# Optimization experiments

Measured on AMD Instinct MI355X. Metric: run time of the kernel, lower is better.

Reference implementation:

```python
import jax, jax.numpy as jnp
import numpy as np

N_VISIBLE = 50000
N_HIDDEN = 5000
N_NODES = N_VISIBLE + N_HIDDEN
N_EDGES = 1_000_000
BATCH = 128


def setup_inputs() -> dict:
    key = jax.random.key(0)
    k1, k2, k3, k4, k5 = jax.random.split(key, 5)
    # parameters, initialized as in the torch module
    linear = 0.05 * (2.0 * jax.random.uniform(k1, (N_NODES,), dtype=jnp.float32) - 1.0)
    quadratic = 5.0 * (2.0 * jax.random.uniform(k2, (N_EDGES,), dtype=jnp.float32) - 1.0)
    # bipartite visible-hidden edges -> CSR-like flat buffers (via segment ids)
    flat_adj = jax.random.randint(k3, (N_EDGES,), 0, N_VISIBLE, dtype=jnp.int32).astype(jnp.int64)  # visible endpoint per edge
    seg_ids = jax.random.randint(k4, (N_EDGES,), 0, N_HIDDEN, dtype=jnp.int32).astype(jnp.int64)    # hidden bin per edge
    flat_j_idx = jnp.arange(N_EDGES, dtype=jnp.int64)  # quadratic coefficient index per flat entry
    hidden_idx = jnp.arange(N_HIDDEN, dtype=jnp.int64) + N_VISIBLE
    # observed spin configurations in {0,1} (mapped to +-1 inside reference)
    s = jax.random.randint(k5, (BATCH, N_NODES), 0, 2, dtype=jnp.int32)
    return {
        "linear": linear,
        "quadratic": quadratic,
        "s": s,
        "flat_adj": flat_adj,
        "flat_j_idx": flat_j_idx,
        "seg_ids": seg_ids,
        "hidden_idx": hidden_idx,
        "n_hidden": N_HIDDEN,
    }


def reference(linear, quadratic, s, flat_adj, flat_j_idx, seg_ids, hidden_idx, n_hidden):
    """Per-hidden-unit effective field + conditional spin expectation.

    eff[b, k] = linear[hidden_idx[k]]
                + sum_{e : seg_ids[e]==k} quadratic[flat_j_idx[e]] * s_pm[b, flat_adj[e]]
    returns tanh(-eff)  (conditional expectation of hidden spins given visibles)
    """
    s_pm = (2 * s - 1).astype(linear.dtype)                 # {0,1} -> {-1,+1}, (B, N)
    w = quadratic[flat_j_idx]                               # (E,)
    contrib = s_pm[:, flat_adj].T * w[:, None]              # (E, B) gathered neighbor terms
    field = jax.ops.segment_sum(contrib, seg_ids, num_segments=n_hidden)  # (K, B)
    eff = field.T + linear[hidden_idx][None, :]             # (B, K)
    return jnp.tanh(-eff)
```

## Files before the change

kernel.cpp:

```cpp
#include <hip/hip_runtime.h>
#include <math.h>
#include <stdint.h>

#define NV 50000
#define NH 5000
#define NN 55000
#define NCB 313
#define BCAP 4096
#define FSLOT 384
#define CHUNK 4096
#define SCAN_N 320


__global__ void __launch_bounds__(256) pack_zero_kernel(
        const int* __restrict__ s, uint32_t* __restrict__ bits,
        uint32_t* __restrict__ coarse_cnt) {
    if (blockIdx.x == 0)
        for (int i = threadIdx.x; i < NCB; i += 256) coarse_cnt[i] = 0u;
    int tid = blockIdx.x * 256 + threadIdx.x;
    int v = tid >> 2;
    int g = tid & 3;
    if (v >= NV) return;
    const int* col = s + (size_t)g * 32 * NN + v;
    uint32_t w = 0;
#pragma unroll
    for (int j = 0; j < 32; ++j)
        w |= (uint32_t)(col[(size_t)j * NN] & 1) << j;
    bits[(size_t)v * 4 + g] = w;
}

__global__ void __launch_bounds__(256) coarse_split_kernel(
        const int4* __restrict__ seg4, const int4* __restrict__ adj4,
        const float4* __restrict__ quad4,
        uint32_t* __restrict__ coarse_cnt, uint2* __restrict__ recs, int E) {
    __shared__ uint32_t hist[SCAN_N];
    __shared__ uint32_t loc[SCAN_N];
    __shared__ uint32_t cur[NCB];
    __shared__ uint32_t gbase[NCB];
    __shared__ __align__(16) uint2 st[CHUNK];
    __shared__ uint32_t dst[CHUNK];
    const int tid = threadIdx.x;
    for (int i = tid; i < SCAN_N; i += 256) hist[i] = 0u;
    __syncthreads();

    const int c0 = blockIdx.x * CHUNK;
    const int nloc = min(CHUNK, E - c0);
    int kreg[16];
#pragma unroll
    for (int j = 0; j < 4; ++j) {
        int t4 = (c0 >> 2) + j * 256 + tid;
        bool ok = t4 < ((c0 + nloc) >> 2);
        int4 sg = ok ? seg4[t4] : make_int4(-1, -1, -1, -1);
        kreg[j * 4 + 0] = sg.x; kreg[j * 4 + 1] = sg.y;
        kreg[j * 4 + 2] = sg.z; kreg[j * 4 + 3] = sg.w;
        if (ok) {
            atomicAdd(&hist[sg.x >> 4], 1u);
            atomicAdd(&hist[sg.y >> 4], 1u);
            atomicAdd(&hist[sg.z >> 4], 1u);
            atomicAdd(&hist[sg.w >> 4], 1u);
        }
    }
    __syncthreads();
    for (int i = tid; i < NCB; i += 256)
        gbase[i] = atomicAdd(&coarse_cnt[i], hist[i]);
    for (int i = tid; i < SCAN_N; i += 256) loc[i] = hist[i];
    __syncthreads();
    for (int d = 1; d < SCAN_N; d <<= 1) {
        uint32_t v0 = 0, v1 = 0;
        int i1 = tid + 256;
        if (tid >= d) v0 = loc[tid - d];
        if (i1 < SCAN_N && i1 >= d) v1 = loc[i1 - d];
        __syncthreads();
        if (tid >= d) loc[tid] += v0;
        if (i1 < SCAN_N && i1 >= d) loc[i1] += v1;
        __syncthreads();
    }
    for (int i = tid; i < NCB; i += 256) cur[i] = loc[i] - hist[i];
    __syncthreads();
#pragma unroll
    for (int j = 0; j < 4; ++j) {
        int t4 = (c0 >> 2) + j * 256 + tid;
        if (t4 < ((c0 + nloc) >> 2)) {
            int4 a = adj4[t4];
            float4 q = quad4[t4];
#pragma unroll
            for (int cmp = 0; cmp < 4; ++cmp) {
                int k = kreg[j * 4 + cmp];
                int v = (cmp == 0) ? a.x : (cmp == 1) ? a.y : (cmp == 2) ? a.z : a.w;
                float w = (cmp == 0) ? q.x : (cmp == 1) ? q.y : (cmp == 2) ? q.z : q.w;
                int bk = k >> 4;
                uint32_t slot = atomicAdd(&cur[bk], 1u);
                uint32_t rank = gbase[bk] + (slot - (loc[bk] - hist[bk]));
                st[slot] = make_uint2((uint32_t)v | ((uint32_t)(k & 15) << 16),
                                      __float_as_uint(w));
                dst[slot] = (rank < BCAP) ? (uint32_t)bk * BCAP + rank : ~0u;
            }
        }
    }
    __syncthreads();
    for (int i = tid; i < nloc; i += 256) {
        uint32_t d = dst[i];
        if (d != ~0u) recs[d] = st[i];
    }
}

__global__ void __launch_bounds__(512) bucket_field_kernel(
        const uint32_t* __restrict__ coarse_cnt, const uint2* __restrict__ recs,
        const uint4* __restrict__ bits4, const float* __restrict__ linear,
        float* __restrict__ out) {
    const int bkt = blockIdx.x;
    const int tid = threadIdx.x;
    __shared__ uint32_t hist[16], off[16], cur[16];
    __shared__ __align__(16) uint2 st[BCAP];
    __shared__ __align__(16) uint32_t rows[4][5][FSLOT];
    __shared__ float part[4][512];

    int cnt = (int)min(coarse_cnt[bkt], (uint32_t)BCAP);
    const uint2* region = recs + (size_t)bkt * BCAP;
    if (tid < 16) hist[tid] = 0u;
    __syncthreads();
    for (int i = tid; i < cnt; i += 512)
        atomicAdd(&hist[(region[i].x >> 16) & 15], 1u);
    __syncthreads();
    if (tid == 0) {
        uint32_t run = 0;
        for (int j = 0; j < 16; ++j) { off[j] = run; cur[j] = run; run += hist[j]; }
    }
    __syncthreads();
    for (int i = tid; i < cnt; i += 512) {
        uint2 r = region[i];
        st[atomicAdd(&cur[(r.x >> 16) & 15], 1u)] = r;
    }
    __syncthreads();

    const int b = tid & 127;
    const int grp = tid >> 7;
    const int bsh = b & 31;
    const int widx = b >> 5;
    for (int rnd = 0; rnd < 4; ++rnd) {
        {
            int kk = grp;
            int kl = rnd * 4 + kk;
            int c = min((int)hist[kl], FSLOT);
            int base = (int)off[kl];
            int T16 = (c + 15) & ~15;
            int lt = b;
            for (int t = c + lt; t < T16; t += 128) rows[kk][4][t] = 0u;
            for (int t = lt; t < c; t += 128) {
                uint2 r = st[base + t];
                uint4 mw = bits4[r.x & 0xFFFFu];
                rows[kk][0][t] = mw.x;
                rows[kk][1][t] = mw.y;
                rows[kk][2][t] = mw.z;
                rows[kk][3][t] = mw.w;
                rows[kk][4][t] = r.y;
            }
        }
        __syncthreads();
#pragma unroll
        for (int kk = 0; kk < 4; ++kk) {
            int kl = rnd * 4 + kk;
            int T16 = (min((int)hist[kl], FSLOT) + 15) & ~15;
            const uint32_t* mrow = rows[kk][widx];
            const uint32_t* wrow = rows[kk][4];
            float a0 = 0.f, a1 = 0.f, a2 = 0.f, a3 = 0.f;
            for (int i = grp * 4; i < T16; i += 16) {
                uint4 mm = *(const uint4*)(mrow + i);
                uint4 ww = *(const uint4*)(wrow + i);
                float f0 = __uint_as_float(ww.x);
                float f1 = __uint_as_float(ww.y);
                float f2 = __uint_as_float(ww.z);
                float f3 = __uint_as_float(ww.w);
                a0 += ((mm.x >> bsh) & 1u) ? f0 : -f0;
                a1 += ((mm.y >> bsh) & 1u) ? f1 : -f1;
                a2 += ((mm.z >> bsh) & 1u) ? f2 : -f2;
                a3 += ((mm.w >> bsh) & 1u) ? f3 : -f3;
            }
            part[kk][tid] = (a0 + a1) + (a2 + a3);
        }
        __syncthreads();
        if (tid < 128) {
            int k0 = bkt * 16 + rnd * 4;
            if (k0 < NH) {
                float4 o;
                float* op = (float*)&o;
#pragma unroll
                for (int kk = 0; kk < 4; ++kk) {
                    float e = part[kk][tid] + part[kk][tid + 128]
                            + part[kk][tid + 256] + part[kk][tid + 384]
                            + linear[NV + k0 + kk];
                    op[kk] = tanhf(-e);
                }
                *(float4*)(out + (size_t)tid * NH + k0) = o;
            }
        }
        __syncthreads();
    }
}

extern "C" void kernel_launch(void* const* d_in, const int* in_sizes, int n_in,
                              void* d_out, int out_size, void* d_ws, size_t ws_size,
                              hipStream_t stream) {
    const float* linear = (const float*)d_in[0];
    const float* quad   = (const float*)d_in[1];
    const int*   s      = (const int*)d_in[2];
    const int*   adj    = (const int*)d_in[3];
    const int*   seg    = (const int*)d_in[5];
    const int E = in_sizes[5];
    float* out = (float*)d_out;

    char* ws = (char*)d_ws;
    uint32_t* bits       = (uint32_t*)(ws);
    uint32_t* coarse_cnt = (uint32_t*)(ws + 800000);
    uint2*    recs       = (uint2*)   (ws + 801280);

    pack_zero_kernel<<<(NV * 4 + 255) / 256, 256, 0, stream>>>(s, bits, coarse_cnt);
    const int nchunk = (E + CHUNK - 1) / CHUNK;
    coarse_split_kernel<<<nchunk, 256, 0, stream>>>(
        (const int4*)seg, (const int4*)adj, (const float4*)quad, coarse_cnt, recs, E);
    bucket_field_kernel<<<NCB, 512, 0, stream>>>(coarse_cnt, recs, (const uint4*)bits,
                                                 linear, out);
}
```

Baseline: 146.9 us.

## Split per-bucket field kernel into quarter blocks and use masked-sum algebra

Result: faster. 133.7 us (-9.0%).

```diff
diff --git a/kernel.cpp b/kernel.cpp
--- a/kernel.cpp
+++ b/kernel.cpp
@@ -7,10 +7,17 @@
 #define NN 55000
 #define NCB 313
 #define BCAP 4096
-#define FSLOT 384
+#define KSLOT 384
 #define CHUNK 4096
-#define SCAN_N 320
-
+
+
+__device__ __forceinline__ uint32_t selmask(uint32_t word, uint32_t bsh) {
+#if __has_builtin(__builtin_amdgcn_sbfe)
+    return (uint32_t)__builtin_amdgcn_sbfe((int)word, bsh, 1u);
+#else
+    return (uint32_t)((int32_t)(word << (31u - bsh)) >> 31);
+#endif
+}
 
 __global__ void __launch_bounds__(256) pack_zero_kernel(
         const int* __restrict__ s, uint32_t* __restrict__ bits,
@@ -33,14 +40,14 @@
         const int4* __restrict__ seg4, const int4* __restrict__ adj4,
         const float4* __restrict__ quad4,
         uint32_t* __restrict__ coarse_cnt, uint2* __restrict__ recs, int E) {
-    __shared__ uint32_t hist[SCAN_N];
-    __shared__ uint32_t loc[SCAN_N];
+    __shared__ uint32_t hist[320];
+    __shared__ uint32_t loc[320];
     __shared__ uint32_t cur[NCB];
     __shared__ uint32_t gbase[NCB];
     __shared__ __align__(16) uint2 st[CHUNK];
     __shared__ uint32_t dst[CHUNK];
     const int tid = threadIdx.x;
-    for (int i = tid; i < SCAN_N; i += 256) hist[i] = 0u;
+    for (int i = tid; i < 320; i += 256) hist[i] = 0u;
     __syncthreads();
 
     const int c0 = blockIdx.x * CHUNK;
@@ -63,16 +70,16 @@
     __syncthreads();
     for (int i = tid; i < NCB; i += 256)
         gbase[i] = atomicAdd(&coarse_cnt[i], hist[i]);
-    for (int i = tid; i < SCAN_N; i += 256) loc[i] = hist[i];
-    __syncthreads();
-    for (int d = 1; d < SCAN_N; d <<= 1) {
+    for (int i = tid; i < 320; i += 256) loc[i] = hist[i];
+    __syncthreads();
+    for (int d = 1; d < 320; d <<= 1) {
         uint32_t v0 = 0, v1 = 0;
         int i1 = tid + 256;
         if (tid >= d) v0 = loc[tid - d];
-        if (i1 < SCAN_N && i1 >= d) v1 = loc[i1 - d];
+        if (i1 < 320 && i1 >= d) v1 = loc[i1 - d];
         __syncthreads();
         if (tid >= d) loc[tid] += v0;
-        if (i1 < SCAN_N && i1 >= d) loc[i1] += v1;
+        if (i1 < 320 && i1 >= d) loc[i1] += v1;
         __syncthreads();
     }
     for (int i = tid; i < NCB; i += 256) cur[i] = loc[i] - hist[i];
@@ -104,94 +111,90 @@
     }
 }
 
-__global__ void __launch_bounds__(512) bucket_field_kernel(
+__global__ void __launch_bounds__(256) quarter_field_kernel(
         const uint32_t* __restrict__ coarse_cnt, const uint2* __restrict__ recs,
         const uint4* __restrict__ bits4, const float* __restrict__ linear,
         float* __restrict__ out) {
-    const int bkt = blockIdx.x;
+    const int x = blockIdx.x;
+    const int j = (x & 7) * 157 + (x >> 3);
+    const int bkt = j >> 2;
+    const int q = j & 3;
+    if (bkt >= NCB) return;
     const int tid = threadIdx.x;
-    __shared__ uint32_t hist[16], off[16], cur[16];
-    __shared__ __align__(16) uint2 st[BCAP];
-    __shared__ __align__(16) uint32_t rows[4][5][FSLOT];
-    __shared__ float part[4][512];
+
+    __shared__ uint32_t cur4[4];
+    __shared__ float swp[4];
+    __shared__ __align__(16) uint2 st4[4][KSLOT];
+    __shared__ __align__(16) uint32_t rows[2][5][KSLOT];
+    __shared__ float part[2][256];
+
+    if (tid < 4) cur4[tid] = 0u;
+    __syncthreads();
 
     int cnt = (int)min(coarse_cnt[bkt], (uint32_t)BCAP);
     const uint2* region = recs + (size_t)bkt * BCAP;
-    if (tid < 16) hist[tid] = 0u;
-    __syncthreads();
-    for (int i = tid; i < cnt; i += 512)
-        atomicAdd(&hist[(region[i].x >> 16) & 15], 1u);
-    __syncthreads();
-    if (tid == 0) {
-        uint32_t run = 0;
-        for (int j = 0; j < 16; ++j) { off[j] = run; cur[j] = run; run += hist[j]; }
-    }
-    __syncthreads();
-    for (int i = tid; i < cnt; i += 512) {
+    for (int i = tid; i < cnt; i += 256) {
         uint2 r = region[i];
-        st[atomicAdd(&cur[(r.x >> 16) & 15], 1u)] = r;
+        int kl = (int)((r.x >> 16) & 15u);
+        if ((kl >> 2) == q) {
+            uint32_t p = atomicAdd(&cur4[kl & 3], 1u);
+            if (p < KSLOT) st4[kl & 3][p] = r;
+        }
     }
     __syncthreads();
 
     const int b = tid & 127;
     const int grp = tid >> 7;
-    const int bsh = b & 31;
+    const uint32_t bsh = (uint32_t)(b & 31);
     const int widx = b >> 5;
-    for (int rnd = 0; rnd < 4; ++rnd) {
-        {
-            int kk = grp;
-            int kl = rnd * 4 + kk;
-            int c = min((int)hist[kl], FSLOT);
-            int base = (int)off[kl];
-            int T16 = (c + 15) & ~15;
-            int lt = b;
-            for (int t = c + lt; t < T16; t += 128) rows[kk][4][t] = 0u;
-            for (int t = lt; t < c; t += 128) {
-                uint2 r = st[base + t];
-                uint4 mw = bits4[r.x & 0xFFFFu];
-                rows[kk][0][t] = mw.x;
-                rows[kk][1][t] = mw.y;
-                rows[kk][2][t] = mw.z;
-                rows[kk][3][t] = mw.w;
-                rows[kk][4][t] = r.y;
-            }
-        }
-        __syncthreads();
-#pragma unroll
-        for (int kk = 0; kk < 4; ++kk) {
-            int kl = rnd * 4 + kk;
-            int T16 = (min((int)hist[kl], FSLOT) + 15) & ~15;
+
+    for (int rnd = 0; rnd < 2; ++rnd) {
+        int kl = rnd * 2 + grp;
+        int c = min((int)cur4[kl], KSLOT);
+        int T8 = (c + 7) & ~7;
+        float sw = 0.f;
+        for (int t = c + b; t < T8; t += 128) rows[grp][4][t] = 0u;
+        for (int t = b; t < c; t += 128) {
+            uint2 r = st4[kl][t];
+            uint4 mw = bits4[r.x & 0xFFFFu];
+            rows[grp][0][t] = mw.x;
+            rows[grp][1][t] = mw.y;
+            rows[grp][2][t] = mw.z;
+            rows[grp][3][t] = mw.w;
+            rows[grp][4][t] = r.y;
+            sw += __uint_as_float(r.y);
+        }
+#pragma unroll
+        for (int off = 32; off; off >>= 1) sw += __shfl_down(sw, off);
+        if ((tid & 63) == 0) swp[tid >> 6] = sw;
+        __syncthreads();
+
+#pragma unroll
+        for (int kk = 0; kk < 2; ++kk) {
+            int T8k = (min((int)cur4[rnd * 2 + kk], KSLOT) + 7) & ~7;
             const uint32_t* mrow = rows[kk][widx];
             const uint32_t* wrow = rows[kk][4];
             float a0 = 0.f, a1 = 0.f, a2 = 0.f, a3 = 0.f;
-            for (int i = grp * 4; i < T16; i += 16) {
+            for (int i = grp * 4; i < T8k; i += 8) {
                 uint4 mm = *(const uint4*)(mrow + i);
                 uint4 ww = *(const uint4*)(wrow + i);
-                float f0 = __uint_as_float(ww.x);
-                float f1 = __uint_as_float(ww.y);
-                float f2 = __uint_as_float(ww.z);
-                float f3 = __uint_as_float(ww.w);
-                a0 += ((mm.x >> bsh) & 1u) ? f0 : -f0;
-                a1 += ((mm.y >> bsh) & 1u) ? f1 : -f1;
-                a2 += ((mm.z >> bsh) & 1u) ? f2 : -f2;
-                a3 += ((mm.w >> bsh) & 1u) ? f3 : -f3;
+                a0 += __uint_as_float(ww.x & selmask(mm.x, bsh));
+                a1 += __uint_as_float(ww.y & selmask(mm.y, bsh));
+                a2 += __uint_as_float(ww.z & selmask(mm.z, bsh));
+                a3 += __uint_as_float(ww.w & selmask(mm.w, bsh));
             }
             part[kk][tid] = (a0 + a1) + (a2 + a3);
         }
         __syncthreads();
         if (tid < 128) {
-            int k0 = bkt * 16 + rnd * 4;
-            if (k0 < NH) {
-                float4 o;
-                float* op = (float*)&o;
-#pragma unroll
-                for (int kk = 0; kk < 4; ++kk) {
-                    float e = part[kk][tid] + part[kk][tid + 128]
-                            + part[kk][tid + 256] + part[kk][tid + 384]
-                            + linear[NV + k0 + kk];
-                    op[kk] = tanhf(-e);
-                }
-                *(float4*)(out + (size_t)tid * NH + k0) = o;
+            int k0 = bkt * 16 + q * 4 + rnd * 2;
+            if (k0 + 1 < NH) {
+                float acc0 = part[0][tid] + part[0][tid + 128];
+                float acc1 = part[1][tid] + part[1][tid + 128];
+                float e0 = 2.f * acc0 - (swp[0] + swp[1]) + linear[NV + k0];
+                float e1 = 2.f * acc1 - (swp[2] + swp[3]) + linear[NV + k0 + 1];
+                float2 o = make_float2(tanhf(-e0), tanhf(-e1));
+                *(float2*)(out + (size_t)tid * NH + k0) = o;
             }
         }
         __syncthreads();
@@ -218,6 +221,6 @@
     const int nchunk = (E + CHUNK - 1) / CHUNK;
     coarse_split_kernel<<<nchunk, 256, 0, stream>>>(
         (const int4*)seg, (const int4*)adj, (const float4*)quad, coarse_cnt, recs, E);
-    bucket_field_kernel<<<NCB, 512, 0, stream>>>(coarse_cnt, recs, (const uint4*)bits,
-                                                 linear, out);
-}
+    quarter_field_kernel<<<1256, 256, 0, stream>>>(coarse_cnt, recs, (const uint4*)bits,
+                                                   linear, out);
+}
```
